# Kernel tuning notes

Hardware: AMD Instinct MI355X
Metric: run time of the kernel (lower is better)

Reference implementation:

```python
import jax, jax.numpy as jnp
import numpy as np

B_SZ, L, H, P = 4, 4096, 1024, 1024
R_MIN, R_MAX, MAX_PHASE = 0.0, 1.0, 6.28


def setup_inputs() -> dict:
    key = jax.random.key(0)
    ks = jax.random.split(key, 8)
    inputs = jax.random.normal(ks[0], (B_SZ, L, H), dtype=jnp.float32)
    # LRU-style init for nu_log/theta_log (keeps |lambda| < 1 so scan is stable)
    u1 = jax.random.uniform(ks[1], (P,))
    nu = -0.5 * jnp.log(u1 * (R_MAX**2 - R_MIN**2) + R_MIN**2)
    nu_log = jnp.log(nu)
    u2 = jax.random.uniform(ks[2], (P,))
    theta_log = jnp.log(MAX_PHASE * u2)
    # variance_scaling(0.5,'fan_out','normal') for B; (1.0,'fan_out','normal') for C
    B_re = jax.random.normal(ks[3], (P, H)) * jnp.sqrt(0.5 / P)
    B_im = jax.random.normal(ks[4], (P, H)) * jnp.sqrt(0.5 / P)
    C_re = jax.random.normal(ks[5], (H, P)) * jnp.sqrt(1.0 / H)
    C_im = jax.random.normal(ks[6], (H, P)) * jnp.sqrt(1.0 / H)
    D = jax.random.normal(ks[7], (H,))
    diag_lambda = jnp.exp(-jnp.exp(nu_log) + 1j * jnp.exp(theta_log))
    gamma_log = jnp.log(jnp.sqrt(1.0 - jnp.abs(diag_lambda) ** 2))
    return {
        "inputs": inputs,
        "nu_log": nu_log.astype(jnp.float32),
        "theta_log": theta_log.astype(jnp.float32),
        "B_re": B_re.astype(jnp.float32),
        "B_im": B_im.astype(jnp.float32),
        "C_re": C_re.astype(jnp.float32),
        "C_im": C_im.astype(jnp.float32),
        "D": D.astype(jnp.float32),
        "gamma_log": gamma_log.astype(jnp.float32),
    }


def reference(inputs, nu_log, theta_log, B_re, B_im, C_re, C_im, D, gamma_log):
    batch_size, input_length, _ = inputs.shape
    Lambda = jnp.exp(-jnp.exp(nu_log) + 1j * jnp.exp(theta_log))  # [P] complex
    Bmat = B_re + 1j * B_im                                        # [P,H]
    Cmat = C_re + 1j * C_im                                        # [H,P]
    gamma = jnp.exp(gamma_log)                                     # [P]
    B_norm = Bmat * gamma[:, None]

    def apply_step(elem_i, elem_j):
        a_i, bu_i = elem_i
        a_j, bu_j = elem_j
        return (a_j * a_i, a_j * bu_i + bu_j)

    Ls = jnp.broadcast_to(Lambda, (batch_size, input_length, Lambda.shape[0]))
    Bu = jnp.einsum('ph,blh->blp', B_norm, inputs.astype(B_norm.dtype))
    _, xs = jax.lax.associative_scan(apply_step, (Ls, Bu), axis=1)
    Cx = jnp.einsum('hp,blp->blh', Cmat, xs).real
    Du = D * inputs
    return Cx + Du
```

## Files before the change

kernel.cpp:

```cpp
#include <hip/hip_runtime.h>
#include <cstdint>
#include <cstddef>

#define MDIM 16384
#define HDIM 1024
#define PDIM 1024
#define LSEQ 4096
#define BSZ  4
#define CHUNK 64
#define NCHUNK 64
#define NBU  2048

typedef float   floatx4  __attribute__((ext_vector_type(4)));
typedef __bf16  bf16x8   __attribute__((ext_vector_type(8)));
typedef unsigned short u16;
typedef unsigned short u16x8 __attribute__((ext_vector_type(8)));

__device__ __forceinline__ u16 f2bf(float f) {
    union { float f; uint32_t u; } v; v.f = f;
    return (u16)((v.u + 0x7fffu + ((v.u >> 16) & 1u)) >> 16);
}
__device__ __forceinline__ float bfu2f(uint32_t bits16) {
    union { float f; uint32_t u; } v; v.u = bits16 << 16; return v.f;
}
__device__ __forceinline__ bf16x8 ldfrag(const u16* p) {
    return __builtin_bit_cast(bf16x8, *(const u16x8*)p);
}
__device__ __forceinline__ void gload16(const u16* g, u16* l) {
    __builtin_amdgcn_global_load_lds(
        (const __attribute__((address_space(1))) uint32_t*)g,
        (__attribute__((address_space(3))) uint32_t*)l, 16, 0, 0);
}

template<int KD>
__device__ __forceinline__ void gemm_core(
    const u16* __restrict__ A, const u16* __restrict__ B,
    int m0, int n0, u16* sA, u16* sB, floatx4 acc[4][4])
{
    const int tid  = threadIdx.x;
    const int wave = tid >> 6, lane = tid & 63;
    const int lrow = lane & 15, lq = lane >> 4;
    const int wm = (wave >> 1) * 64, wn = (wave & 1) * 64;
    const int srow   = lane >> 3;
    const int schunk = (lane & 7) ^ srow;

    const u16* aptr = A + (size_t)(m0 + wave * 32 + srow) * KD + schunk * 8;
    const u16* bptr = B + (size_t)(n0 + wave * 32 + srow) * KD + schunk * 8;
    u16* sAw = sA + wave * 32 * 64;
    u16* sBw = sB + wave * 32 * 64;

    for (int k0 = 0; k0 < KD; k0 += 64) {
        #pragma unroll
        for (int i = 0; i < 4; ++i) {
            gload16(aptr + (size_t)i * 8 * KD + k0, sAw + i * 8 * 64);
            gload16(bptr + (size_t)i * 8 * KD + k0, sBw + i * 8 * 64);
        }
        __syncthreads();
        #pragma unroll
        for (int s = 0; s < 2; ++s) {
            bf16x8 af[4], bfr[4];
            #pragma unroll
            for (int mt = 0; mt < 4; ++mt) {
                int r = wm + mt * 16 + lrow;
                af[mt] = ldfrag(sA + r * 64 + (((s * 4 + lq) ^ (r & 7)) * 8));
            }
            #pragma unroll
            for (int nt = 0; nt < 4; ++nt) {
                int r = wn + nt * 16 + lrow;
                bfr[nt] = ldfrag(sB + r * 64 + (((s * 4 + lq) ^ (r & 7)) * 8));
            }
            #pragma unroll
            for (int mt = 0; mt < 4; ++mt)
                #pragma unroll
                for (int nt = 0; nt < 4; ++nt)
                    acc[mt][nt] = __builtin_amdgcn_mfma_f32_16x16x32_bf16(
                        af[mt], bfr[nt], acc[mt][nt], 0, 0, 0);
        }
        __syncthreads();
    }
}

#define ST 136
__global__ __launch_bounds__(256) void gemm_bu_k(
    const u16* __restrict__ A, const u16* __restrict__ B, u16* __restrict__ O)
{
    __shared__ u16 smem[128 * ST];
    u16* sA = smem;
    u16* sB = smem + 128 * 64;
    floatx4 acc[4][4] = {};
    const int d = blockIdx.x;
    const int xcd = d & 7, s = d >> 3;
    const int m0 = (xcd * 16 + (s >> 4)) * 128;
    const int n0 = (s & 15) * 128;
    gemm_core<HDIM>(A, B, m0, n0, sA, sB, acc);

    const int tid = threadIdx.x, wave = tid >> 6, lane = tid & 63;
    const int lrow = lane & 15, lq = lane >> 4;
    const int wm = (wave >> 1) * 64, wn = (wave & 1) * 64;

    #pragma unroll
    for (int nt = 0; nt < 4; ++nt) {
        int col = wn + nt * 16 + lrow;
        #pragma unroll
        for (int mt = 0; mt < 4; ++mt)
            #pragma unroll
            for (int r = 0; r < 4; ++r) {
                int row = wm + mt * 16 + lq * 4 + r;
                smem[row * ST + col] = f2bf(acc[mt][nt][r]);
            }
    }
    __syncthreads();

    const int col = (tid & 15) * 8;
    const int rb  = tid >> 4;
    #pragma unroll
    for (int j = 0; j < 8; ++j) {
        int row = rb + j * 16;
        *(u16x8*)(O + (size_t)(m0 + row) * NBU + n0 + col) =
            *(const u16x8*)(smem + row * ST + col);
    }
}

__global__ __launch_bounds__(256) void gemm_out_k(
    const u16* __restrict__ A, const u16* __restrict__ B,
    const float* __restrict__ Dv, const u16* __restrict__ Ubf,
    float* __restrict__ O)
{
    __shared__ u16 sA[128 * 64];
    __shared__ u16 sB[128 * 64];
    floatx4 acc[4][4] = {};
    const int d = blockIdx.x;
    const int xcd = d & 7, s = d >> 3;
    const int m0 = (xcd * 16 + (s >> 3)) * 128;
    const int n0 = (s & 7) * 128;
    gemm_core<NBU>(A, B, m0, n0, sA, sB, acc);

    const int tid = threadIdx.x, wave = tid >> 6, lane = tid & 63;
    const int lrow = lane & 15, lq = lane >> 4;
    const int wm = (wave >> 1) * 64, wn = (wave & 1) * 64;
    #pragma unroll
    for (int nt = 0; nt < 4; ++nt) {
        int col = n0 + wn + nt * 16 + lrow;
        float dval = Dv[col];
        #pragma unroll
        for (int mt = 0; mt < 4; ++mt)
            #pragma unroll
            for (int r = 0; r < 4; ++r) {
                int row = m0 + wm + mt * 16 + lq * 4 + r;
                size_t o = (size_t)row * HDIM + col;
                O[o] = acc[mt][nt][r] + dval * bfu2f(Ubf[o]);
            }
    }
}

__global__ __launch_bounds__(256) void prep_all(
    const float* __restrict__ U, u16* __restrict__ Ubf,
    const float* __restrict__ Bre, const float* __restrict__ Bim,
    const float* __restrict__ gamma_log, u16* __restrict__ Bcomb,
    const float* __restrict__ Cre, const float* __restrict__ Cim,
    u16* __restrict__ Bcbf)
{
    const int bid = blockIdx.x;
    if (bid < 8192) {
        size_t i = ((size_t)bid * 256 + threadIdx.x) * 8;
        float4 a = *(const float4*)(U + i);
        float4 b = *(const float4*)(U + i + 4);
        u16x8 w;
        w[0]=f2bf(a.x); w[1]=f2bf(a.y); w[2]=f2bf(a.z); w[3]=f2bf(a.w);
        w[4]=f2bf(b.x); w[5]=f2bf(b.y); w[6]=f2bf(b.z); w[7]=f2bf(b.w);
        *(u16x8*)(Ubf + i) = w;
    } else if (bid < 9216) {
        int t = (bid - 8192) * 256 + threadIdx.x;
        int n = t >> 7;
        int h = (t & 127) * 8;
        int p = n >> 1, sflag = n & 1;
        const float* src = (sflag ? Bim : Bre) + (size_t)p * HDIM + h;
        float g = expf(gamma_log[p]);
        float4 a = *(const float4*)src;
        float4 b = *(const float4*)(src + 4);
        u16x8 w;
        w[0]=f2bf(a.x*g); w[1]=f2bf(a.y*g); w[2]=f2bf(a.z*g); w[3]=f2bf(a.w*g);
        w[4]=f2bf(b.x*g); w[5]=f2bf(b.y*g); w[6]=f2bf(b.z*g); w[7]=f2bf(b.w*g);
        *(u16x8*)(Bcomb + (size_t)n * HDIM + h) = w;
    } else {
        int t = (bid - 9216) * 256 + threadIdx.x;
        int h = t >> 8;
        int k = (t & 255) * 4;
        float4 cr = *(const float4*)(Cre + (size_t)h * PDIM + k);
        float4 ci = *(const float4*)(Cim + (size_t)h * PDIM + k);
        u16x8 w;
        w[0]=f2bf(cr.x); w[1]=f2bf(-ci.x);
        w[2]=f2bf(cr.y); w[3]=f2bf(-ci.y);
        w[4]=f2bf(cr.z); w[5]=f2bf(-ci.z);
        w[6]=f2bf(cr.w); w[7]=f2bf(-ci.w);
        *(u16x8*)(Bcbf + (size_t)h * NBU + 2 * k) = w;
    }
}

__global__ __launch_bounds__(256) void scan_passA(
    const uint32_t* __restrict__ BuC,
    const float* __restrict__ nu_log, const float* __restrict__ theta_log,
    float* __restrict__ endC)
{
    int tid = blockIdx.x * 256 + threadIdx.x;
    int p0 = (tid & 511) * 2;
    int c  = (tid >> 9) & (NCHUNK - 1);
    int b  = tid >> 15;
    float nu0 = expf(nu_log[p0]),     th0 = expf(theta_log[p0]);
    float nu1 = expf(nu_log[p0 + 1]), th1 = expf(theta_log[p0 + 1]);
    float el0 = expf(-nu0), el1 = expf(-nu1);
    float lr0 = el0 * cosf(th0), li0 = el0 * sinf(th0);
    float lr1 = el1 * cosf(th1), li1 = el1 * sinf(th1);
    const uint32_t* src = BuC + (size_t)(b * LSEQ + c * CHUNK) * PDIM + p0;
    float xr0 = 0.f, xi0 = 0.f, xr1 = 0.f, xi1 = 0.f;
    #pragma unroll 8
    for (int t = 0; t < CHUNK; ++t) {
        uint2 v = *(const uint2*)(src + (size_t)t * PDIM);
        float br0 = bfu2f(v.x & 0xffffu), bi0 = bfu2f(v.x >> 16);
        float br1 = bfu2f(v.y & 0xffffu), bi1 = bfu2f(v.y >> 16);
        float nr0 = fmaf(lr0, xr0, fmaf(-li0, xi0, br0));
        float ni0 = fmaf(lr0, xi0, fmaf(li0, xr0, bi0));
        float nr1 = fmaf(lr1, xr1, fmaf(-li1, xi1, br1));
        float ni1 = fmaf(lr1, xi1, fmaf(li1, xr1, bi1));
        xr0 = nr0; xi0 = ni0; xr1 = nr1; xi1 = ni1;
    }
    float4 e; e.x = xr0; e.y = xi0; e.z = xr1; e.w = xi1;
    *(float4*)(endC + (((size_t)b * NCHUNK + c) * PDIM + p0) * 2) = e;
}

__global__ __launch_bounds__(256) void scan_passB(
    const float* __restrict__ endC,
    const float* __restrict__ nu_log, const float* __restrict__ theta_log,
    float* __restrict__ carryC)
{
    int tid = blockIdx.x * 256 + threadIdx.x;
    int p0 = (tid & 511) * 2;
    int b  = tid >> 9;
    float nu0 = expf(nu_log[p0]),     th0 = expf(theta_log[p0]);
    float nu1 = expf(nu_log[p0 + 1]), th1 = expf(theta_log[p0 + 1]);
    float e0 = expf(-nu0 * (float)CHUNK), a0 = th0 * (float)CHUNK;
    float e1 = expf(-nu1 * (float)CHUNK), a1 = th1 * (float)CHUNK;
    float Lr0 = e0 * cosf(a0), Li0 = e0 * sinf(a0);
    float Lr1 = e1 * cosf(a1), Li1 = e1 * sinf(a1);
    float gr0 = 0.f, gi0 = 0.f, gr1 = 0.f, gi1 = 0.f;
    for (int g = 0; g < 8; ++g) {
        float4 e[8];
        #pragma unroll
        for (int j = 0; j < 8; ++j)
            e[j] = *(const float4*)(endC + (((size_t)b * NCHUNK + g * 8 + j) * PDIM + p0) * 2);
        #pragma unroll
        for (int j = 0; j < 8; ++j) {
            size_t idx = (((size_t)b * NCHUNK + g * 8 + j) * PDIM + p0) * 2;
            float4 go; go.x = gr0; go.y = gi0; go.z = gr1; go.w = gi1;
            *(float4*)(carryC + idx) = go;
            float nr0 = fmaf(Lr0, gr0, fmaf(-Li0, gi0, e[j].x));
            float ni0 = fmaf(Lr0, gi0, fmaf(Li0, gr0, e[j].y));
            float nr1 = fmaf(Lr1, gr1, fmaf(-Li1, gi1, e[j].z));
            float ni1 = fmaf(Lr1, gi1, fmaf(Li1, gr1, e[j].w));
            gr0 = nr0; gi0 = ni0; gr1 = nr1; gi1 = ni1;
        }
    }
}

__global__ __launch_bounds__(256) void scan_passC(
    uint32_t* __restrict__ BuC,
    const float* __restrict__ nu_log, const float* __restrict__ theta_log,
    const float* __restrict__ carryC)
{
    int tid = blockIdx.x * 256 + threadIdx.x;
    int p0 = (tid & 511) * 2;
    int c  = (tid >> 9) & (NCHUNK - 1);
    int b  = tid >> 15;
    float nu0 = expf(nu_log[p0]),     th0 = expf(theta_log[p0]);
    float nu1 = expf(nu_log[p0 + 1]), th1 = expf(theta_log[p0 + 1]);
    float el0 = expf(-nu0), el1 = expf(-nu1);
    float lr0 = el0 * cosf(th0), li0 = el0 * sinf(th0);
    float lr1 = el1 * cosf(th1), li1 = el1 * sinf(th1);
    float4 g = *(const float4*)(carryC + (((size_t)b * NCHUNK + c) * PDIM + p0) * 2);
    float xr0 = g.x, xi0 = g.y, xr1 = g.z, xi1 = g.w;
    uint32_t* ptr = BuC + (size_t)(b * LSEQ + c * CHUNK) * PDIM + p0;
    #pragma unroll 8
    for (int t = 0; t < CHUNK; ++t) {
        uint32_t* q = ptr + (size_t)t * PDIM;
        uint2 v = *(const uint2*)q;
        float br0 = bfu2f(v.x & 0xffffu), bi0 = bfu2f(v.x >> 16);
        float br1 = bfu2f(v.y & 0xffffu), bi1 = bfu2f(v.y >> 16);
        float nr0 = fmaf(lr0, xr0, fmaf(-li0, xi0, br0));
        float ni0 = fmaf(lr0, xi0, fmaf(li0, xr0, bi0));
        float nr1 = fmaf(lr1, xr1, fmaf(-li1, xi1, br1));
        float ni1 = fmaf(lr1, xi1, fmaf(li1, xr1, bi1));
        xr0 = nr0; xi0 = ni0; xr1 = nr1; xi1 = ni1;
        uint2 o;
        o.x = (uint32_t)f2bf(xr0) | ((uint32_t)f2bf(xi0) << 16);
        o.y = (uint32_t)f2bf(xr1) | ((uint32_t)f2bf(xi1) << 16);
        *(uint2*)q = o;
    }
}

extern "C" void kernel_launch(void* const* d_in, const int* in_sizes, int n_in,
                              void* d_out, int out_size, void* d_ws, size_t ws_size,
                              hipStream_t stream)
{
    (void)in_sizes; (void)n_in; (void)out_size; (void)ws_size;
    const float* U         = (const float*)d_in[0];
    const float* nu_log    = (const float*)d_in[1];
    const float* theta_log = (const float*)d_in[2];
    const float* B_re      = (const float*)d_in[3];
    const float* B_im      = (const float*)d_in[4];
    const float* C_re      = (const float*)d_in[5];
    const float* C_im      = (const float*)d_in[6];
    const float* Dv        = (const float*)d_in[7];
    const float* gamma_log = (const float*)d_in[8];
    float* out = (float*)d_out;

    char* ws = (char*)d_ws;
    u16*   BuC    = (u16*)ws;
    u16*   Ubf    = (u16*)(ws + (size_t)64 * 1024 * 1024);
    u16*   Bcomb  = (u16*)(ws + (size_t)96 * 1024 * 1024);
    u16*   Bcbf   = (u16*)(ws + (size_t)100 * 1024 * 1024);
    float* endC   = (float*)(ws + (size_t)104 * 1024 * 1024);
    float* carryC = (float*)(ws + (size_t)106 * 1024 * 1024);

    prep_all<<<8192 + 1024 + 1024, 256, 0, stream>>>(
        U, Ubf, B_re, B_im, gamma_log, Bcomb, C_re, C_im, Bcbf);

    gemm_bu_k<<<2048, 256, 0, stream>>>(Ubf, Bcomb, BuC);

    scan_passA<<<(BSZ * NCHUNK * PDIM / 2) / 256, 256, 0, stream>>>(
        (const uint32_t*)BuC, nu_log, theta_log, endC);
    scan_passB<<<(BSZ * PDIM / 2) / 256, 256, 0, stream>>>(endC, nu_log, theta_log, carryC);
    scan_passC<<<(BSZ * NCHUNK * PDIM / 2) / 256, 256, 0, stream>>>(
        (uint32_t*)BuC, nu_log, theta_log, carryC);

    gemm_out_k<<<1024, 256, 0, stream>>>(BuC, Bcbf, Dv, Ubf, out);
}
```

Measured before the change: 342.2 us.

## Replace GEMM cores with 256x256 double-buffered 8-wave pipelined kernel

Both GEMMs move from a 128x128 tile with 4 waves and single-buffered LDS to a 256x256 tile with 8 waves. The new core double-buffers LDS and interleaves global-to-LDS loads with MFMA phases, using explicit vmcnt waits, barriers and setprio. The goal is to hide memory latency and raise arithmetic intensity per loaded byte. In exchange it uses 128KB of LDS and more registers, launches fewer blocks (512 and 256), and adds a swizzled LDS staging path for the bf16 output store.

After: 352.9 us. +3.1%, slower.

```diff
diff --git a/kernel.cpp b/kernel.cpp
--- a/kernel.cpp
+++ b/kernel.cpp
@@ -32,123 +32,214 @@
         (__attribute__((address_space(3))) uint32_t*)l, 16, 0, 0);
 }
 
+#define BARRIER() do { \
+    asm volatile("" ::: "memory"); \
+    __builtin_amdgcn_sched_barrier(0); \
+    __builtin_amdgcn_s_barrier(); \
+    __builtin_amdgcn_sched_barrier(0); \
+    asm volatile("" ::: "memory"); \
+} while (0)
+
+#define WAITV(N_) do { \
+    __builtin_amdgcn_sched_barrier(0); \
+    asm volatile("s_waitcnt vmcnt(" #N_ ")" ::: "memory"); \
+    __builtin_amdgcn_sched_barrier(0); \
+} while (0)
+
+template<int MH>
+__device__ __forceinline__ void ldA(const u16* buf, int aBase, int c0, int c1,
+                                    bf16x8 (&aF)[4][2]) {
+    #pragma unroll
+    for (int mf = 0; mf < 4; ++mf) {
+        const u16* p = buf + aBase + (MH * 4 + mf) * 1024;
+        aF[mf][0] = ldfrag(p + c0);
+        aF[mf][1] = ldfrag(p + c1);
+    }
+}
+template<int NH>
+__device__ __forceinline__ void ldB(const u16* buf, int bBase, int c0, int c1,
+                                    bf16x8 (&bF)[2][2]) {
+    #pragma unroll
+    for (int j = 0; j < 2; ++j) {
+        const u16* p = buf + bBase + (NH * 2 + j) * 1024;
+        bF[j][0] = ldfrag(p + c0);
+        bF[j][1] = ldfrag(p + c1);
+    }
+}
+template<int MH, int NH>
+__device__ __forceinline__ void doMFMA(bf16x8 (&aF)[4][2], bf16x8 (&bF)[2][2],
+                                       floatx4 (&acc)[8][4]) {
+    __builtin_amdgcn_s_setprio(1);
+    #pragma unroll
+    for (int s = 0; s < 2; ++s)
+        #pragma unroll
+        for (int mf = 0; mf < 4; ++mf)
+            #pragma unroll
+            for (int j = 0; j < 2; ++j)
+                acc[MH * 4 + mf][NH * 2 + j] =
+                    __builtin_amdgcn_mfma_f32_16x16x32_bf16(
+                        aF[mf][s], bF[j][s], acc[MH * 4 + mf][NH * 2 + j],
+                        0, 0, 0);
+    __builtin_amdgcn_s_setprio(0);
+}
+
 template<int KD>
-__device__ __forceinline__ void gemm_core(
+__device__ __forceinline__ void gemm256_core(
     const u16* __restrict__ A, const u16* __restrict__ B,
-    int m0, int n0, u16* sA, u16* sB, floatx4 acc[4][4])
+    int m0, int n0, u16* smem, floatx4 (&acc)[8][4])
 {
     const int tid  = threadIdx.x;
     const int wave = tid >> 6, lane = tid & 63;
     const int lrow = lane & 15, lq = lane >> 4;
-    const int wm = (wave >> 1) * 64, wn = (wave & 1) * 64;
-    const int srow   = lane >> 3;
-    const int schunk = (lane & 7) ^ srow;
-
-    const u16* aptr = A + (size_t)(m0 + wave * 32 + srow) * KD + schunk * 8;
-    const u16* bptr = B + (size_t)(n0 + wave * 32 + srow) * KD + schunk * 8;
-    u16* sAw = sA + wave * 32 * 64;
-    u16* sBw = sB + wave * 32 * 64;
-
-    for (int k0 = 0; k0 < KD; k0 += 64) {
-        #pragma unroll
-        for (int i = 0; i < 4; ++i) {
-            gload16(aptr + (size_t)i * 8 * KD + k0, sAw + i * 8 * 64);
-            gload16(bptr + (size_t)i * 8 * KD + k0, sBw + i * 8 * 64);
-        }
-        __syncthreads();
-        #pragma unroll
-        for (int s = 0; s < 2; ++s) {
-            bf16x8 af[4], bfr[4];
-            #pragma unroll
-            for (int mt = 0; mt < 4; ++mt) {
-                int r = wm + mt * 16 + lrow;
-                af[mt] = ldfrag(sA + r * 64 + (((s * 4 + lq) ^ (r & 7)) * 8));
-            }
-            #pragma unroll
-            for (int nt = 0; nt < 4; ++nt) {
-                int r = wn + nt * 16 + lrow;
-                bfr[nt] = ldfrag(sB + r * 64 + (((s * 4 + lq) ^ (r & 7)) * 8));
-            }
-            #pragma unroll
-            for (int mt = 0; mt < 4; ++mt)
-                #pragma unroll
-                for (int nt = 0; nt < 4; ++nt)
-                    acc[mt][nt] = __builtin_amdgcn_mfma_f32_16x16x32_bf16(
-                        af[mt], bfr[nt], acc[mt][nt], 0, 0, 0);
-        }
-        __syncthreads();
-    }
-}
-
-#define ST 136
-__global__ __launch_bounds__(256) void gemm_bu_k(
+    const int wm = wave >> 2, wn = wave & 3;
+    const int axr = lrow & 7;
+    const int c0 = (lq ^ axr) * 8;
+    const int c1 = ((4 + lq) ^ axr) * 8;
+    const int aBase = (wm * 128 + lrow) * 64;
+    const int bBase = (wn * 64  + lrow) * 64;
+    const int srow = tid >> 3;
+    const int schk = (tid & 7) ^ (srow & 7);
+    const u16* aptr = A + (size_t)(m0 + srow) * KD + schk * 8;
+    const u16* bptr = B + (size_t)(n0 + srow) * KD + schk * 8;
+    u16* const sA0 = smem;
+    u16* const sB0 = smem + 16384;
+    u16* const sA1 = smem + 32768;
+    u16* const sB1 = smem + 49152;
+    const int lw = wave * 512;
+
+    bf16x8 aF[4][2], bF[2][2];
+
+    #pragma unroll
+    for (int i = 0; i < 4; ++i) {
+        gload16(aptr + (size_t)i * 64 * KD, sA0 + i * 4096 + lw);
+        gload16(bptr + (size_t)i * 64 * KD, sB0 + i * 4096 + lw);
+    }
+    WAITV(0);
+    BARRIER();
+
+    #define STG(i_, k_, dA_, dB_) do { \
+        gload16(aptr + (size_t)(i_) * 64 * KD + (k_), (dA_) + (i_) * 4096 + lw); \
+        gload16(bptr + (size_t)(i_) * 64 * KD + (k_), (dB_) + (i_) * 4096 + lw); \
+    } while (0)
+
+    for (int k = 0; k < KD; k += 128) {
+        const int k1 = k + 64, k2 = k + 128;
+        STG(0, k1, sA1, sB1);
+        WAITV(2);
+        BARRIER();
+        ldA<0>(sA0, aBase, c0, c1, aF);
+        ldB<0>(sB0, bBase, c0, c1, bF);
+        doMFMA<0, 0>(aF, bF, acc);
+        BARRIER();
+        ldB<1>(sB0, bBase, c0, c1, bF);
+        STG(1, k1, sA1, sB1);
+        BARRIER();
+        doMFMA<0, 1>(aF, bF, acc);
+        BARRIER();
+        ldA<1>(sA0, aBase, c0, c1, aF);
+        STG(2, k1, sA1, sB1);
+        BARRIER();
+        doMFMA<1, 1>(aF, bF, acc);
+        BARRIER();
+        ldB<0>(sB0, bBase, c0, c1, bF);
+        STG(3, k1, sA1, sB1);
+        BARRIER();
+        doMFMA<1, 0>(aF, bF, acc);
+        BARRIER();
+
+        if (k2 < KD) { STG(0, k2, sA0, sB0); WAITV(2); } else { WAITV(0); }
+        BARRIER();
+        ldA<0>(sA1, aBase, c0, c1, aF);
+        ldB<0>(sB1, bBase, c0, c1, bF);
+        doMFMA<0, 0>(aF, bF, acc);
+        BARRIER();
+
+        ldB<1>(sB1, bBase, c0, c1, bF);
+        if (k2 < KD) STG(1, k2, sA0, sB0);
+        BARRIER();
+        doMFMA<0, 1>(aF, bF, acc);
+        BARRIER();
+
+        ldA<1>(sA1, aBase, c0, c1, aF);
+        if (k2 < KD) STG(2, k2, sA0, sB0);
+        BARRIER();
+        doMFMA<1, 1>(aF, bF, acc);
+        BARRIER();
+
+        ldB<0>(sB1, bBase, c0, c1, bF);
+        if (k2 < KD) STG(3, k2, sA0, sB0);
+        BARRIER();
+        doMFMA<1, 0>(aF, bF, acc);
+        BARRIER();
+    }
+    #undef STG
+}
+
+__global__ __launch_bounds__(512, 2) void gemm_bu_k(
     const u16* __restrict__ A, const u16* __restrict__ B, u16* __restrict__ O)
 {
-    __shared__ u16 smem[128 * ST];
-    u16* sA = smem;
-    u16* sB = smem + 128 * 64;
-    floatx4 acc[4][4] = {};
+    __shared__ __align__(16) u16 smem[65536];
+    floatx4 acc[8][4] = {};
     const int d = blockIdx.x;
     const int xcd = d & 7, s = d >> 3;
-    const int m0 = (xcd * 16 + (s >> 4)) * 128;
-    const int n0 = (s & 15) * 128;
-    gemm_core<HDIM>(A, B, m0, n0, sA, sB, acc);
+    const int m0 = (xcd * 8 + (s >> 3)) * 256;
+    const int n0 = (s & 7) * 256;
+    gemm256_core<HDIM>(A, B, m0, n0, smem, acc);
 
     const int tid = threadIdx.x, wave = tid >> 6, lane = tid & 63;
     const int lrow = lane & 15, lq = lane >> 4;
-    const int wm = (wave >> 1) * 64, wn = (wave & 1) * 64;
-
-    #pragma unroll
-    for (int nt = 0; nt < 4; ++nt) {
-        int col = wn + nt * 16 + lrow;
-        #pragma unroll
-        for (int mt = 0; mt < 4; ++mt)
+    const int wm = wave >> 2, wn = wave & 3;
+    u16* lwp = smem + wave * 4096;
+    #pragma unroll
+    for (int mh = 0; mh < 2; ++mh) {
+        #pragma unroll
+        for (int mfl = 0; mfl < 4; ++mfl)
             #pragma unroll
-            for (int r = 0; r < 4; ++r) {
-                int row = wm + mt * 16 + lq * 4 + r;
-                smem[row * ST + col] = f2bf(acc[mt][nt][r]);
-            }
-    }
-    __syncthreads();
-
-    const int col = (tid & 15) * 8;
-    const int rb  = tid >> 4;
-    #pragma unroll
-    for (int j = 0; j < 8; ++j) {
-        int row = rb + j * 16;
-        *(u16x8*)(O + (size_t)(m0 + row) * NBU + n0 + col) =
-            *(const u16x8*)(smem + row * ST + col);
-    }
-}
-
-__global__ __launch_bounds__(256) void gemm_out_k(
+            for (int nf = 0; nf < 4; ++nf)
+                #pragma unroll
+                for (int r = 0; r < 4; ++r) {
+                    int rowl = mfl * 16 + lq * 4 + r;
+                    int cpos = (nf * 2 + (lrow >> 3)) ^ (rowl & 7);
+                    lwp[rowl * 64 + cpos * 8 + (lrow & 7)] =
+                        f2bf(acc[mh * 4 + mfl][nf][r]);
+                }
+        int grow = m0 + wm * 128 + mh * 64 + lane;
+        #pragma unroll
+        for (int j = 0; j < 8; ++j) {
+            int cpos = j ^ (lane & 7);
+            *(u16x8*)(O + (size_t)grow * NBU + n0 + wn * 64 + j * 8) =
+                *(const u16x8*)(lwp + lane * 64 + cpos * 8);
+        }
+    }
+}
+
+__global__ __launch_bounds__(512, 2) void gemm_out_k(
     const u16* __restrict__ A, const u16* __restrict__ B,
     const float* __restrict__ Dv, const u16* __restrict__ Ubf,
     float* __restrict__ O)
 {
-    __shared__ u16 sA[128 * 64];
-    __shared__ u16 sB[128 * 64];
-    floatx4 acc[4][4] = {};
+    __shared__ __align__(16) u16 smem[65536];
+    floatx4 acc[8][4] = {};
     const int d = blockIdx.x;
     const int xcd = d & 7, s = d >> 3;
-    const int m0 = (xcd * 16 + (s >> 3)) * 128;
-    const int n0 = (s & 7) * 128;
-    gemm_core<NBU>(A, B, m0, n0, sA, sB, acc);
+    const int m0 = (xcd * 8 + (s >> 2)) * 256;
+    const int n0 = (s & 3) * 256;
+    gemm256_core<NBU>(A, B, m0, n0, smem, acc);
 
     const int tid = threadIdx.x, wave = tid >> 6, lane = tid & 63;
     const int lrow = lane & 15, lq = lane >> 4;
-    const int wm = (wave >> 1) * 64, wn = (wave & 1) * 64;
-    #pragma unroll
-    for (int nt = 0; nt < 4; ++nt) {
-        int col = n0 + wn + nt * 16 + lrow;
+    const int wm = wave >> 2, wn = wave & 3;
+    #pragma unroll
+    for (int nf = 0; nf < 4; ++nf) {
+        int col = n0 + wn * 64 + nf * 16 + lrow;
         float dval = Dv[col];
         #pragma unroll
-        for (int mt = 0; mt < 4; ++mt)
+        for (int mf = 0; mf < 8; ++mf)
             #pragma unroll
             for (int r = 0; r < 4; ++r) {
-                int row = m0 + wm + mt * 16 + lq * 4 + r;
+                int row = m0 + wm * 128 + mf * 16 + lq * 4 + r;
                 size_t o = (size_t)row * HDIM + col;
-                O[o] = acc[mt][nt][r] + dval * bfu2f(Ubf[o]);
+                O[o] = acc[mf][nf][r] + dval * bfu2f(Ubf[o]);
             }
     }
 }
@@ -324,7 +415,7 @@
     prep_all<<<8192 + 1024 + 1024, 256, 0, stream>>>(
         U, Ubf, B_re, B_im, gamma_log, Bcomb, C_re, C_im, Bcbf);
 
-    gemm_bu_k<<<2048, 256, 0, stream>>>(Ubf, Bcomb, BuC);
+    gemm_bu_k<<<512, 512, 0, stream>>>(Ubf, Bcomb, BuC);
 
     scan_passA<<<(BSZ * NCHUNK * PDIM / 2) / 256, 256, 0, stream>>>(
         (const uint32_t*)BuC, nu_log, theta_log, endC);
@@ -332,5 +423,5 @@
     scan_passC<<<(BSZ * NCHUNK * PDIM / 2) / 256, 256, 0, stream>>>(
         (uint32_t*)BuC, nu_log, theta_log, carryC);
 
-    gemm_out_k<<<1024, 256, 0, stream>>>(BuC, Bcbf, Dv, Ubf, out);
-}
+    gemm_out_k<<<256, 512, 0, stream>>>(BuC, Bcbf, Dv, Ubf, out);
+}
```

## Rewrite output GEMM as 256x256 tile with 512 threads and double-buffered LDS pipeline

Applied to the files above, without the earlier changes.

The output GEMM (BuC x Ccomb, K=2048) moves from 128x128 tiles with 256 threads to 256x256 tiles with 8 waves. Each wave computes 128x64. Global-to-LDS loads are double-buffered, with explicit vmcnt waits, barriers and setprio interleaving the prefetch against the MFMA phases. This is meant to raise operand reuse and hide load latency. The cost is only 256 blocks, which may underfill the CUs, plus a 128KB LDS footprint and heavy register pressure.

After: 351.2 us. 1.03x slower.

```diff
diff --git a/kernel.cpp b/kernel.cpp
--- a/kernel.cpp
+++ b/kernel.cpp
@@ -32,8 +32,22 @@
         (__attribute__((address_space(3))) uint32_t*)l, 16, 0, 0);
 }
 
+#define BARRIER() do { \
+    asm volatile("" ::: "memory"); \
+    __builtin_amdgcn_sched_barrier(0); \
+    __builtin_amdgcn_s_barrier(); \
+    __builtin_amdgcn_sched_barrier(0); \
+    asm volatile("" ::: "memory"); \
+} while (0)
+
+#define WAITV(N_) do { \
+    __builtin_amdgcn_sched_barrier(0); \
+    asm volatile("s_waitcnt vmcnt(" #N_ ")" ::: "memory"); \
+    __builtin_amdgcn_sched_barrier(0); \
+} while (0)
+
 template<int KD>
-__device__ __forceinline__ void gemm_core(
+__device__ __forceinline__ void gemm_core128(
     const u16* __restrict__ A, const u16* __restrict__ B,
     int m0, int n0, u16* sA, u16* sB, floatx4 acc[4][4])
 {
@@ -78,6 +92,127 @@
         }
         __syncthreads();
     }
+}
+
+template<int MH>
+__device__ __forceinline__ void ldA(const u16* buf, int aBase, int c0, int c1,
+                                    bf16x8 (&aF)[4][2]) {
+    #pragma unroll
+    for (int mf = 0; mf < 4; ++mf) {
+        const u16* p = buf + aBase + (MH * 4 + mf) * 1024;
+        aF[mf][0] = ldfrag(p + c0);
+        aF[mf][1] = ldfrag(p + c1);
+    }
+}
+template<int NH>
+__device__ __forceinline__ void ldB(const u16* buf, int bBase, int c0, int c1,
+                                    bf16x8 (&bF)[2][2]) {
+    #pragma unroll
+    for (int j = 0; j < 2; ++j) {
+        const u16* p = buf + bBase + (NH * 2 + j) * 1024;
+        bF[j][0] = ldfrag(p + c0);
+        bF[j][1] = ldfrag(p + c1);
+    }
+}
+template<int MH, int NH>
+__device__ __forceinline__ void doMFMA(bf16x8 (&aF)[4][2], bf16x8 (&bF)[2][2],
+                                       floatx4 (&acc)[8][4]) {
+    __builtin_amdgcn_s_setprio(1);
+    #pragma unroll
+    for (int s = 0; s < 2; ++s)
+        #pragma unroll
+        for (int mf = 0; mf < 4; ++mf)
+            #pragma unroll
+            for (int j = 0; j < 2; ++j)
+                acc[MH * 4 + mf][NH * 2 + j] =
+                    __builtin_amdgcn_mfma_f32_16x16x32_bf16(
+                        aF[mf][s], bF[j][s], acc[MH * 4 + mf][NH * 2 + j],
+                        0, 0, 0);
+    __builtin_amdgcn_s_setprio(0);
+}
+
+template<int KD>
+__device__ __forceinline__ void gemm256_deep(
+    const u16* __restrict__ A, const u16* __restrict__ B,
+    int m0, int n0, u16* smem, floatx4 (&acc)[8][4])
+{
+    const int tid  = threadIdx.x;
+    const int wave = tid >> 6, lane = tid & 63;
+    const int lrow = lane & 15, lq = lane >> 4;
+    const int wm = wave >> 2, wn = wave & 3;
+    const int axr = lrow & 7;
+    const int c0 = (lq ^ axr) * 8;
+    const int c1 = ((4 + lq) ^ axr) * 8;
+    const int aBase = (wm * 128 + lrow) * 64;
+    const int bBase = (wn * 64  + lrow) * 64;
+    const int srow = tid >> 3;
+    const int schk = (tid & 7) ^ (srow & 7);
+    const u16* aptr = A + (size_t)(m0 + srow) * KD + schk * 8;
+    const u16* bptr = B + (size_t)(n0 + srow) * KD + schk * 8;
+    const int lw = wave * 512;
+
+    u16* const a0 = smem;          u16* const b0 = smem + 16384;
+    u16* const a1 = smem + 32768;  u16* const b1 = smem + 49152;
+
+    bf16x8 aF[4][2], bFa[2][2], bFb[2][2];
+    const int NT = KD / 64;
+
+    #define STGA(d_, h_, k_) do { \
+        gload16(aptr + (size_t)((h_) * 2 + 0) * 64 * KD + (k_), (d_) + ((h_) * 2 + 0) * 4096 + lw); \
+        gload16(aptr + (size_t)((h_) * 2 + 1) * 64 * KD + (k_), (d_) + ((h_) * 2 + 1) * 4096 + lw); \
+    } while (0)
+    #define STGB(d_, h_, k_) do { \
+        gload16(bptr + (size_t)((h_) * 2 + 0) * 64 * KD + (k_), (d_) + ((h_) * 2 + 0) * 4096 + lw); \
+        gload16(bptr + (size_t)((h_) * 2 + 1) * 64 * KD + (k_), (d_) + ((h_) * 2 + 1) * 4096 + lw); \
+    } while (0)
+
+    STGA(a0, 0, 0); STGA(a0, 1, 0);
+    STGB(b0, 0, 0); STGB(b0, 1, 0);
+    STGB(b1, 0, 64);
+    STGA(a1, 0, 64); STGA(a1, 1, 64);
+    WAITV(6);
+    BARRIER();
+
+    #define TILE(u_, cA_, cB_, nB_) do { \
+         \
+        ldA<0>(cA_, aBase, c0, c1, aF); \
+        ldB<0>(cB_, bBase, c0, c1, bFa); \
+        if ((u_) + 1 < NT) STGB(nB_, 1, ((u_) + 1) * 64); \
+        BARRIER(); \
+        doMFMA<0, 0>(aF, bFa, acc); \
+        BARRIER(); \
+         \
+        ldB<1>(cB_, bBase, c0, c1, bFb); \
+        BARRIER(); \
+        doMFMA<0, 1>(aF, bFb, acc); \
+        BARRIER(); \
+         \
+        ldA<1>(cA_, aBase, c0, c1, aF); \
+        if ((u_) + 2 < NT) STGB(cB_, 0, ((u_) + 2) * 64); \
+        BARRIER(); \
+        doMFMA<1, 1>(aF, bFb, acc); \
+        BARRIER(); \
+         \
+         \
+        if ((u_) + 2 < NT) { \
+            STGA(cA_, 0, ((u_) + 2) * 64); \
+            STGA(cA_, 1, ((u_) + 2) * 64); \
+            WAITV(6); \
+        } else { \
+            WAITV(0); \
+        } \
+        BARRIER(); \
+        doMFMA<1, 0>(aF, bFa, acc); \
+        BARRIER(); \
+    } while (0)
+
+    for (int up = 0; up < NT / 2; ++up) {
+        TILE(2 * up,     a0, b0, b1);
+        TILE(2 * up + 1, a1, b1, b0);
+    }
+    #undef TILE
+    #undef STGA
+    #undef STGB
 }
 
 #define ST 136
@@ -92,7 +227,7 @@
     const int xcd = d & 7, s = d >> 3;
     const int m0 = (xcd * 16 + (s >> 4)) * 128;
     const int n0 = (s & 15) * 128;
-    gemm_core<HDIM>(A, B, m0, n0, sA, sB, acc);
+    gemm_core128<HDIM>(A, B, m0, n0, sA, sB, acc);
 
     const int tid = threadIdx.x, wave = tid >> 6, lane = tid & 63;
     const int lrow = lane & 15, lq = lane >> 4;
@@ -121,34 +256,33 @@
     }
 }
 
-__global__ __launch_bounds__(256) void gemm_out_k(
+__global__ __launch_bounds__(512, 2) void gemm_out_k(
     const u16* __restrict__ A, const u16* __restrict__ B,
     const float* __restrict__ Dv, const u16* __restrict__ Ubf,
     float* __restrict__ O)
 {
-    __shared__ u16 sA[128 * 64];
-    __shared__ u16 sB[128 * 64];
-    floatx4 acc[4][4] = {};
+    __shared__ __align__(16) u16 smem[65536];
+    floatx4 acc[8][4] = {};
     const int d = blockIdx.x;
     const int xcd = d & 7, s = d >> 3;
-    const int m0 = (xcd * 16 + (s >> 3)) * 128;
-    const int n0 = (s & 7) * 128;
-    gemm_core<NBU>(A, B, m0, n0, sA, sB, acc);
+    const int m0 = (xcd * 8 + (s >> 2)) * 256;
+    const int n0 = (s & 3) * 256;
+    gemm256_deep<NBU>(A, B, m0, n0, smem, acc);
 
     const int tid = threadIdx.x, wave = tid >> 6, lane = tid & 63;
     const int lrow = lane & 15, lq = lane >> 4;
-    const int wm = (wave >> 1) * 64, wn = (wave & 1) * 64;
-    #pragma unroll
-    for (int nt = 0; nt < 4; ++nt) {
-        int col = n0 + wn + nt * 16 + lrow;
+    const int wm = wave >> 2, wn = wave & 3;
+    #pragma unroll
+    for (int nf = 0; nf < 4; ++nf) {
+        int col = n0 + wn * 64 + nf * 16 + lrow;
         float dval = Dv[col];
         #pragma unroll
-        for (int mt = 0; mt < 4; ++mt)
+        for (int mf = 0; mf < 8; ++mf)
             #pragma unroll
             for (int r = 0; r < 4; ++r) {
-                int row = m0 + wm + mt * 16 + lq * 4 + r;
+                int row = m0 + wm * 128 + mf * 16 + lq * 4 + r;
                 size_t o = (size_t)row * HDIM + col;
-                O[o] = acc[mt][nt][r] + dval * bfu2f(Ubf[o]);
+                O[o] = acc[mf][nf][r] + dval * bfu2f(Ubf[o]);
             }
     }
 }
@@ -332,5 +466,5 @@
     scan_passC<<<(BSZ * NCHUNK * PDIM / 2) / 256, 256, 0, stream>>>(
         (uint32_t*)BuC, nu_log, theta_log, carryC);
 
-    gemm_out_k<<<1024, 256, 0, stream>>>(BuC, Bcbf, Dv, Ubf, out);
-}
+    gemm_out_k<<<256, 512, 0, stream>>>(BuC, Bcbf, Dv, Ubf, out);
+}
```

## Fuse three-pass chunked scan into single-pass decoupled lookback scan

Applied to the files above, without the earlier changes.

Replaces the separate chunk-reduce, carry-propagate and apply passes with one kernel. Each block takes a dynamic chunk id from an atomic counter, publishes its local aggregate, then looks back over earlier chunks' aggregates or inclusive prefixes using spin-waits. It then rescans its chunk with the resolved carry. This removes two kernel launches and the serial carry kernel, but adds a small control-zeroing kernel, cross-block spin waits, and reuses the Bcomb workspace region for the control flags.

Measured after the change: 505.3 us. +47.7%, slower.

```diff
diff --git a/kernel.cpp b/kernel.cpp
--- a/kernel.cpp
+++ b/kernel.cpp
@@ -33,7 +33,7 @@
 }
 
 template<int KD>
-__device__ __forceinline__ void gemm_core(
+__device__ __forceinline__ void gemm_core128(
     const u16* __restrict__ A, const u16* __restrict__ B,
     int m0, int n0, u16* sA, u16* sB, floatx4 acc[4][4])
 {
@@ -92,7 +92,7 @@
     const int xcd = d & 7, s = d >> 3;
     const int m0 = (xcd * 16 + (s >> 4)) * 128;
     const int n0 = (s & 15) * 128;
-    gemm_core<HDIM>(A, B, m0, n0, sA, sB, acc);
+    gemm_core128<HDIM>(A, B, m0, n0, sA, sB, acc);
 
     const int tid = threadIdx.x, wave = tid >> 6, lane = tid & 63;
     const int lrow = lane & 15, lq = lane >> 4;
@@ -133,7 +133,7 @@
     const int xcd = d & 7, s = d >> 3;
     const int m0 = (xcd * 16 + (s >> 3)) * 128;
     const int n0 = (s & 7) * 128;
-    gemm_core<NBU>(A, B, m0, n0, sA, sB, acc);
+    gemm_core128<NBU>(A, B, m0, n0, sA, sB, acc);
 
     const int tid = threadIdx.x, wave = tid >> 6, lane = tid & 63;
     const int lrow = lane & 15, lq = lane >> 4;
@@ -197,25 +197,47 @@
     }
 }
 
-__global__ __launch_bounds__(256) void scan_passA(
-    const uint32_t* __restrict__ BuC,
+__global__ __launch_bounds__(256) void zero_ctl(uint32_t* __restrict__ ctl)
+{
+    ctl[threadIdx.x] = 0u;
+    ctl[256 + threadIdx.x] = 0u;
+    ctl[512 + threadIdx.x] = 0u;
+    ctl[768 + threadIdx.x] = 0u;
+}
+
+__global__ __launch_bounds__(256) void scan_fused(
+    uint32_t* __restrict__ BuC,
     const float* __restrict__ nu_log, const float* __restrict__ theta_log,
-    float* __restrict__ endC)
-{
-    int tid = blockIdx.x * 256 + threadIdx.x;
-    int p0 = (tid & 511) * 2;
-    int c  = (tid >> 9) & (NCHUNK - 1);
-    int b  = tid >> 15;
+    uint32_t* __restrict__ ctl,
+    float* __restrict__ agg,
+    float* __restrict__ inc)
+{
+    __shared__ int s_vid;
+    if (threadIdx.x == 0)
+        s_vid = (int)atomicAdd(&ctl[0], 1u);
+    __syncthreads();
+    const int vid   = s_vid;
+    const int c     = vid >> 3, chain = vid & 7;
+    const int b     = chain >> 1, half = chain & 1;
+    const int thr   = threadIdx.x;
+    const int p0    = half * 512 + thr * 2;
+
     float nu0 = expf(nu_log[p0]),     th0 = expf(theta_log[p0]);
     float nu1 = expf(nu_log[p0 + 1]), th1 = expf(theta_log[p0 + 1]);
     float el0 = expf(-nu0), el1 = expf(-nu1);
     float lr0 = el0 * cosf(th0), li0 = el0 * sinf(th0);
     float lr1 = el1 * cosf(th1), li1 = el1 * sinf(th1);
-    const uint32_t* src = BuC + (size_t)(b * LSEQ + c * CHUNK) * PDIM + p0;
+    float e640 = expf(-nu0 * (float)CHUNK), a640 = th0 * (float)CHUNK;
+    float e641 = expf(-nu1 * (float)CHUNK), a641 = th1 * (float)CHUNK;
+    float Lr0 = e640 * cosf(a640), Li0 = e640 * sinf(a640);
+    float Lr1 = e641 * cosf(a641), Li1 = e641 * sinf(a641);
+
+    uint32_t* base = BuC + (size_t)(b * LSEQ + c * CHUNK) * PDIM + p0;
+
     float xr0 = 0.f, xi0 = 0.f, xr1 = 0.f, xi1 = 0.f;
     #pragma unroll 8
     for (int t = 0; t < CHUNK; ++t) {
-        uint2 v = *(const uint2*)(src + (size_t)t * PDIM);
+        uint2 v = *(const uint2*)(base + (size_t)t * PDIM);
         float br0 = bfu2f(v.x & 0xffffu), bi0 = bfu2f(v.x >> 16);
         float br1 = bfu2f(v.y & 0xffffu), bi1 = bfu2f(v.y >> 16);
         float nr0 = fmaf(lr0, xr0, fmaf(-li0, xi0, br0));
@@ -224,64 +246,61 @@
         float ni1 = fmaf(lr1, xi1, fmaf(li1, xr1, bi1));
         xr0 = nr0; xi0 = ni0; xr1 = nr1; xi1 = ni1;
     }
-    float4 e; e.x = xr0; e.y = xi0; e.z = xr1; e.w = xi1;
-    *(float4*)(endC + (((size_t)b * NCHUNK + c) * PDIM + p0) * 2) = e;
-}
-
-__global__ __launch_bounds__(256) void scan_passB(
-    const float* __restrict__ endC,
-    const float* __restrict__ nu_log, const float* __restrict__ theta_log,
-    float* __restrict__ carryC)
-{
-    int tid = blockIdx.x * 256 + threadIdx.x;
-    int p0 = (tid & 511) * 2;
-    int b  = tid >> 9;
-    float nu0 = expf(nu_log[p0]),     th0 = expf(theta_log[p0]);
-    float nu1 = expf(nu_log[p0 + 1]), th1 = expf(theta_log[p0 + 1]);
-    float e0 = expf(-nu0 * (float)CHUNK), a0 = th0 * (float)CHUNK;
-    float e1 = expf(-nu1 * (float)CHUNK), a1 = th1 * (float)CHUNK;
-    float Lr0 = e0 * cosf(a0), Li0 = e0 * sinf(a0);
-    float Lr1 = e1 * cosf(a1), Li1 = e1 * sinf(a1);
-    float gr0 = 0.f, gi0 = 0.f, gr1 = 0.f, gi1 = 0.f;
-    for (int g = 0; g < 8; ++g) {
-        float4 e[8];
-        #pragma unroll
-        for (int j = 0; j < 8; ++j)
-            e[j] = *(const float4*)(endC + (((size_t)b * NCHUNK + g * 8 + j) * PDIM + p0) * 2);
-        #pragma unroll
-        for (int j = 0; j < 8; ++j) {
-            size_t idx = (((size_t)b * NCHUNK + g * 8 + j) * PDIM + p0) * 2;
-            float4 go; go.x = gr0; go.y = gi0; go.z = gr1; go.w = gi1;
-            *(float4*)(carryC + idx) = go;
-            float nr0 = fmaf(Lr0, gr0, fmaf(-Li0, gi0, e[j].x));
-            float ni0 = fmaf(Lr0, gi0, fmaf(Li0, gr0, e[j].y));
-            float nr1 = fmaf(Lr1, gr1, fmaf(-Li1, gi1, e[j].z));
-            float ni1 = fmaf(Lr1, gi1, fmaf(Li1, gr1, e[j].w));
-            gr0 = nr0; gi0 = ni0; gr1 = nr1; gi1 = ni1;
+
+    {
+        float* ag = agg + (size_t)vid * 1024 + thr * 4;
+        __hip_atomic_store(&ag[0], xr0, __ATOMIC_RELAXED, __HIP_MEMORY_SCOPE_AGENT);
+        __hip_atomic_store(&ag[1], xi0, __ATOMIC_RELAXED, __HIP_MEMORY_SCOPE_AGENT);
+        __hip_atomic_store(&ag[2], xr1, __ATOMIC_RELAXED, __HIP_MEMORY_SCOPE_AGENT);
+        __hip_atomic_store(&ag[3], xi1, __ATOMIC_RELAXED, __HIP_MEMORY_SCOPE_AGENT);
+    }
+    __syncthreads();
+    if (threadIdx.x == 0)
+        __hip_atomic_store(&ctl[1 + vid], 1u, __ATOMIC_RELEASE, __HIP_MEMORY_SCOPE_AGENT);
+
+    float cr0 = 0.f, ci0 = 0.f, cr1 = 0.f, ci1 = 0.f;
+    if (c > 0) {
+        float pr0 = 1.f, pi0 = 0.f, pr1 = 1.f, pi1 = 0.f;
+        int d = 1;
+        while (true) {
+            const int pv = vid - 8 * d;
+            uint32_t f;
+            while ((f = __hip_atomic_load(&ctl[1 + pv], __ATOMIC_ACQUIRE,
+                                          __HIP_MEMORY_SCOPE_AGENT)) == 0u)
+                __builtin_amdgcn_s_sleep(1);
+            const float* src = (f == 2u ? inc : agg) + (size_t)pv * 1024 + thr * 4;
+            float vr0 = __hip_atomic_load(&src[0], __ATOMIC_RELAXED, __HIP_MEMORY_SCOPE_AGENT);
+            float vi0 = __hip_atomic_load(&src[1], __ATOMIC_RELAXED, __HIP_MEMORY_SCOPE_AGENT);
+            float vr1 = __hip_atomic_load(&src[2], __ATOMIC_RELAXED, __HIP_MEMORY_SCOPE_AGENT);
+            float vi1 = __hip_atomic_load(&src[3], __ATOMIC_RELAXED, __HIP_MEMORY_SCOPE_AGENT);
+            cr0 += pr0 * vr0 - pi0 * vi0;  ci0 += pr0 * vi0 + pi0 * vr0;
+            cr1 += pr1 * vr1 - pi1 * vi1;  ci1 += pr1 * vi1 + pi1 * vr1;
+            if (f == 2u || pv < 8) break;
+            float t0 = pr0 * Lr0 - pi0 * Li0; pi0 = pr0 * Li0 + pi0 * Lr0; pr0 = t0;
+            float t1 = pr1 * Lr1 - pi1 * Li1; pi1 = pr1 * Li1 + pi1 * Lr1; pr1 = t1;
+            ++d;
         }
     }
-}
-
-__global__ __launch_bounds__(256) void scan_passC(
-    uint32_t* __restrict__ BuC,
-    const float* __restrict__ nu_log, const float* __restrict__ theta_log,
-    const float* __restrict__ carryC)
-{
-    int tid = blockIdx.x * 256 + threadIdx.x;
-    int p0 = (tid & 511) * 2;
-    int c  = (tid >> 9) & (NCHUNK - 1);
-    int b  = tid >> 15;
-    float nu0 = expf(nu_log[p0]),     th0 = expf(theta_log[p0]);
-    float nu1 = expf(nu_log[p0 + 1]), th1 = expf(theta_log[p0 + 1]);
-    float el0 = expf(-nu0), el1 = expf(-nu1);
-    float lr0 = el0 * cosf(th0), li0 = el0 * sinf(th0);
-    float lr1 = el1 * cosf(th1), li1 = el1 * sinf(th1);
-    float4 g = *(const float4*)(carryC + (((size_t)b * NCHUNK + c) * PDIM + p0) * 2);
-    float xr0 = g.x, xi0 = g.y, xr1 = g.z, xi1 = g.w;
-    uint32_t* ptr = BuC + (size_t)(b * LSEQ + c * CHUNK) * PDIM + p0;
+
+    {
+        float gr0 = fmaf(Lr0, cr0, fmaf(-Li0, ci0, xr0));
+        float gi0 = fmaf(Lr0, ci0, fmaf(Li0, cr0, xi0));
+        float gr1 = fmaf(Lr1, cr1, fmaf(-Li1, ci1, xr1));
+        float gi1 = fmaf(Lr1, ci1, fmaf(Li1, cr1, xi1));
+        float* ic = inc + (size_t)vid * 1024 + thr * 4;
+        __hip_atomic_store(&ic[0], gr0, __ATOMIC_RELAXED, __HIP_MEMORY_SCOPE_AGENT);
+        __hip_atomic_store(&ic[1], gi0, __ATOMIC_RELAXED, __HIP_MEMORY_SCOPE_AGENT);
+        __hip_atomic_store(&ic[2], gr1, __ATOMIC_RELAXED, __HIP_MEMORY_SCOPE_AGENT);
+        __hip_atomic_store(&ic[3], gi1, __ATOMIC_RELAXED, __HIP_MEMORY_SCOPE_AGENT);
+    }
+    __syncthreads();
+    if (threadIdx.x == 0)
+        __hip_atomic_store(&ctl[1 + vid], 2u, __ATOMIC_RELEASE, __HIP_MEMORY_SCOPE_AGENT);
+
+    xr0 = cr0; xi0 = ci0; xr1 = cr1; xi1 = ci1;
     #pragma unroll 8
     for (int t = 0; t < CHUNK; ++t) {
-        uint32_t* q = ptr + (size_t)t * PDIM;
+        uint32_t* q = base + (size_t)t * PDIM;
         uint2 v = *(const uint2*)q;
         float br0 = bfu2f(v.x & 0xffffu), bi0 = bfu2f(v.x >> 16);
         float br1 = bfu2f(v.y & 0xffffu), bi1 = bfu2f(v.y >> 16);
@@ -314,23 +333,22 @@
     float* out = (float*)d_out;
 
     char* ws = (char*)d_ws;
-    u16*   BuC    = (u16*)ws;
-    u16*   Ubf    = (u16*)(ws + (size_t)64 * 1024 * 1024);
-    u16*   Bcomb  = (u16*)(ws + (size_t)96 * 1024 * 1024);
-    u16*   Bcbf   = (u16*)(ws + (size_t)100 * 1024 * 1024);
-    float* endC   = (float*)(ws + (size_t)104 * 1024 * 1024);
-    float* carryC = (float*)(ws + (size_t)106 * 1024 * 1024);
+    u16*      BuC   = (u16*)ws;
+    u16*      Ubf   = (u16*)(ws + (size_t)64 * 1024 * 1024);
+    u16*      Bcomb = (u16*)(ws + (size_t)96 * 1024 * 1024);
+    u16*      Bcbf  = (u16*)(ws + (size_t)100 * 1024 * 1024);
+    float*    agg   = (float*)(ws + (size_t)104 * 1024 * 1024);
+    float*    inc   = (float*)(ws + (size_t)106 * 1024 * 1024);
+    uint32_t* ctl   = (uint32_t*)(ws + (size_t)96 * 1024 * 1024);
 
     prep_all<<<8192 + 1024 + 1024, 256, 0, stream>>>(
         U, Ubf, B_re, B_im, gamma_log, Bcomb, C_re, C_im, Bcbf);
 
     gemm_bu_k<<<2048, 256, 0, stream>>>(Ubf, Bcomb, BuC);
 
-    scan_passA<<<(BSZ * NCHUNK * PDIM / 2) / 256, 256, 0, stream>>>(
-        (const uint32_t*)BuC, nu_log, theta_log, endC);
-    scan_passB<<<(BSZ * PDIM / 2) / 256, 256, 0, stream>>>(endC, nu_log, theta_log, carryC);
-    scan_passC<<<(BSZ * NCHUNK * PDIM / 2) / 256, 256, 0, stream>>>(
-        (uint32_t*)BuC, nu_log, theta_log, carryC);
+    zero_ctl<<<1, 256, 0, stream>>>(ctl);
+    scan_fused<<<BSZ * NCHUNK * 2, 256, 0, stream>>>(
+        (uint32_t*)BuC, nu_log, theta_log, ctl, agg, inc);
 
     gemm_out_k<<<1024, 256, 0, stream>>>(BuC, Bcbf, Dv, Ubf, out);
 }
```
